# Kernel tuning notes

Measured on AMD Instinct MI355X. Metric: run time of the kernel, lower is better.

The kernel has to match this reference:

```python
import jax, jax.numpy as jnp
import numpy as np

T, B, I, H, K = 200, 2048, 128, 128, 4


def setup_inputs() -> dict:
    key = jax.random.key(0)
    ks = jax.random.split(key, 7)
    inputs = jax.random.normal(ks[0], (T, B, I), jnp.float32)
    lengths = jax.random.randint(ks[1], (B,), 1, T + 1, jnp.int32)
    si = 1.0 / np.sqrt(I)
    sh = 1.0 / np.sqrt(H)
    w0 = jax.random.uniform(ks[2], (H,), jnp.float32, -sh, sh)      # Linear(H,1,bias=False)
    w1_w = jax.random.uniform(ks[3], (H, I), jnp.float32, -si, si)  # Linear(I,H)
    w1_b = jax.random.uniform(ks[4], (H,), jnp.float32, -si, si)
    w2_w = jax.random.uniform(ks[5], (H, I), jnp.float32, -si, si)  # Linear(I,H,bias=False)
    w3_w = jax.random.uniform(ks[6], (H, I), jnp.float32, -si, si)  # Linear(I,H,bias=False)
    return dict(inputs=inputs, lengths=lengths, label_len=4,
                w0=w0, w1_w=w1_w, w1_b=w1_b, w2_w=w2_w, w3_w=w3_w)


def reference(inputs, lengths, label_len, w0, w1_w, w1_b, w2_w, w3_w):
    # inputs: [T, B, I] time-major padded sequences; lengths: [B]
    T_, B_, _ = inputs.shape
    Kl = label_len
    dt = inputs.dtype
    # packed semantics: padded positions are exactly zero
    valid = (jnp.arange(T_)[:, None] < lengths[None, :])  # [T, B]
    x = inputs * valid[..., None].astype(dt)
    x1 = x @ w1_w.T + w1_b                                 # [T, B, H]
    x2 = x @ w2_w.T                                        # [T, B, H]
    # running mean m_s[t] = mean(inputs[:t+1]) (zeros at padding, as in torch)
    m_s = jnp.cumsum(x, axis=0) / jnp.arange(1, T_ + 1, dtype=dt)[:, None, None]
    # labeled timesteps: last min(L, label_len) steps of each sequence
    start = jnp.maximum(lengths - Kl, 0)                   # [B]
    t_lab = start[:, None] + jnp.arange(Kl)[None, :]       # [B, K]
    lab_valid = t_lab < lengths[:, None]                   # [B, K]
    t_c = jnp.minimum(t_lab, T_ - 1)
    b_idx = jnp.arange(B_)[:, None]
    x2_lab = x2[t_c, b_idx]                                # [B, K, H]
    wms_lab = m_s[t_c, b_idx] @ w3_w.T                     # [B, K, H]
    c = x2_lab + wms_lab                                   # [B, K, H]
    # att[b,k,s] = w0 . sigmoid(x1[s,b] + x2[t_k,b] + wms[t_k,b])
    att = jnp.einsum('sbkh,h->bks',
                     jax.nn.sigmoid(x1[:, :, None, :] + c[None, :, :, :]), w0)
    causal = (jnp.arange(T_)[None, None, :] <= t_lab[:, :, None]) & lab_valid[:, :, None]
    att = att * causal.astype(dt)                          # [B, K, T]
    h = jnp.einsum('bks,sbh->bkh', att, x1) + x2_lab       # [B, K, H]
    return h * lab_valid[..., None].astype(dt)
```

## Files before the change

kernel.cpp:

```cpp
#include <hip/hip_runtime.h>
#include <stdint.h>

#define T_DIM 200
#define B_DIM 2048
#define I_DIM 128
#define H_DIM 128
#define TS    32

typedef float  f32x4  __attribute__((ext_vector_type(4)));
typedef __bf16 bf16x8 __attribute__((ext_vector_type(8)));

union BF8 { ushort4 u2[2]; bf16x8 v; };

static __device__ __forceinline__ unsigned short f2bf(float f) {
    union { __bf16 b; unsigned short u; } c; c.b = (__bf16)f; return c.u;
}
static __device__ __forceinline__ float bf2f(unsigned short s) {
    union { unsigned u; float f; } c; c.u = ((unsigned)s) << 16;
    return c.f;
}
static __device__ __forceinline__ ushort4 cvt4(float4 v) {
    return make_ushort4(f2bf(v.x), f2bf(v.y), f2bf(v.z), f2bf(v.w));
}

static __device__ __forceinline__ int ekbase(int h) {
    return (h << 3) ^ ((h >> 4) << 3);
}

__global__ __launch_bounds__(256, 4) void fused_kernel(
    const float* __restrict__ x, const int* __restrict__ lengths,
    const float* __restrict__ w0, const float* __restrict__ w1,
    const float* __restrict__ b1, const float* __restrict__ w2,
    const float* __restrict__ w3, float* __restrict__ out,
    unsigned* __restrict__ wq)
{
    __shared__ __align__(16) unsigned short xs[TS][136];
    __shared__ __align__(16) unsigned short x1s[TS][130];
    __shared__ __align__(16) float attp[TS][36];
    __shared__ __align__(16) float attk[TS][4];
    __shared__ __align__(16) float ektS2[H_DIM * 8];
    __shared__ __align__(16) float x2ls[4][H_DIM];
    __shared__ __align__(16) unsigned short axl[4][136];
    __shared__ __align__(16) unsigned short ams[4][136];
    __shared__ int b_sh;

    const int tid  = threadIdx.x;
    const int lane = tid & 63;
    const int wv   = tid >> 6;
    const int l15  = lane & 15;
    const int quad = lane >> 4;

    if (tid < 128) ektS2[ekbase(tid) + 4] = w0[tid];

    bf16x8 bfr[2][4];
    float  bias[2];
    #pragma unroll
    for (int nt = 0; nt < 2; ++nt) {
        const int n = wv * 32 + nt * 16 + l15;
        bias[nt] = b1[n];
        #pragma unroll
        for (int ks = 0; ks < 4; ++ks) {
            const int kc = ks * 32 + quad * 8;
            const float4 p0 = *(const float4*)(w1 + (size_t)n * I_DIM + kc);
            const float4 p1 = *(const float4*)(w1 + (size_t)n * I_DIM + kc + 4);
            BF8 t;
            t.u2[0] = cvt4(p0);
            t.u2[1] = cvt4(p1);
            bfr[nt][ks] = t.v;
        }
    }

    const int sr0 = tid >> 5;
    const int sf4 = tid & 31;
    const int i   = tid & 127;
    const int hcol = tid & 127;
    const int half = tid >> 7;
    const int rE  = wv * 8 + (lane >> 3);
    const int hE0 = (lane & 7) * 16;

    int bprev = -1;
    for (;;) {
        int b;
        if (wq) {
            if (tid == 0) b_sh = (int)atomicAdd(wq, 1u);
            __syncthreads();
            b = b_sh;
        } else {
            if (bprev >= 0) break;
            b = blockIdx.x;
        }
        if (b >= B_DIM) break;
        bprev = b;

        const int L     = lengths[b];
        const int start = (L > 4) ? (L - 4) : 0;
        const int nv    = (L < 4) ? L : 4;

        const float* xp = x + (size_t)b * I_DIM + i;
        float v0 = 0.f, v1 = 0.f, v2 = 0.f, v3 = 0.f;
        if (tid < 128) {
            v0 = xp[(size_t)(start + 0) * (B_DIM * I_DIM)];
            v1 = xp[(size_t)(start + 1) * (B_DIM * I_DIM)];
            v2 = xp[(size_t)(start + 2) * (B_DIM * I_DIM)];
            v3 = xp[(size_t)(start + 3) * (B_DIM * I_DIM)];
        }

        {
            const float* xq = x + (size_t)b * I_DIM + sf4 * 4;
            const size_t RS = (size_t)B_DIM * I_DIM;
            f32x4 s0 = (f32x4){0.f, 0.f, 0.f, 0.f};
            f32x4 s1 = s0, s2 = s0, s3 = s0;
            int t = sr0;
            for (; t + 24 < start; t += 32) {
                s0 += *(const f32x4*)(xq + (size_t)(t     ) * RS);
                s1 += *(const f32x4*)(xq + (size_t)(t +  8) * RS);
                s2 += *(const f32x4*)(xq + (size_t)(t + 16) * RS);
                s3 += *(const f32x4*)(xq + (size_t)(t + 24) * RS);
            }
            for (; t < start; t += 8)
                s0 += *(const f32x4*)(xq + (size_t)t * RS);
            const f32x4 s = (s0 + s1) + (s2 + s3);
            float* psum = &attp[0][0];
            *(f32x4*)&psum[sr0 * 132 + sf4 * 4] = s;
        }
        __syncthreads();

        if (tid < 128) {
            const float* psum = &attp[0][0];
            float p = 0.f;
            #pragma unroll
            for (int g = 0; g < 8; ++g) p += psum[g * 132 + i];
            const float p0 = p + v0, p1 = p0 + v1, p2 = p1 + v2, p3 = p2 + v3;
            axl[0][i] = f2bf(v0); axl[1][i] = f2bf(v1);
            axl[2][i] = f2bf(v2); axl[3][i] = f2bf(v3);
            ams[0][i] = f2bf(p0 / (float)(start + 1));
            ams[1][i] = f2bf(p1 / (float)(start + 2));
            ams[2][i] = f2bf(p2 / (float)(start + 3));
            ams[3][i] = f2bf(p3 / (float)(start + 4));
        }
        __syncthreads();

        #pragma unroll
        for (int nt = 0; nt < 2; ++nt) {
            const int n = wv * 32 + nt * 16 + l15;
            f32x4 c1 = (f32x4){0.f, 0.f, 0.f, 0.f};
            f32x4 c2 = (f32x4){0.f, 0.f, 0.f, 0.f};
            #pragma unroll
            for (int ks = 0; ks < 4; ++ks) {
                const int kc = ks * 32 + quad * 8;
                const bf16x8 a1 = *(const bf16x8*)&axl[l15 & 3][kc];
                const bf16x8 a2 = *(const bf16x8*)&ams[l15 & 3][kc];
                const float4 q0 = *(const float4*)(w2 + (size_t)n * I_DIM + kc);
                const float4 q1 = *(const float4*)(w2 + (size_t)n * I_DIM + kc + 4);
                const float4 r0 = *(const float4*)(w3 + (size_t)n * I_DIM + kc);
                const float4 r1 = *(const float4*)(w3 + (size_t)n * I_DIM + kc + 4);
                BF8 bw2, bw3;
                bw2.u2[0] = cvt4(q0); bw2.u2[1] = cvt4(q1);
                bw3.u2[0] = cvt4(r0); bw3.u2[1] = cvt4(r1);
                c1 = __builtin_amdgcn_mfma_f32_16x16x32_bf16(a1, bw2.v, c1, 0, 0, 0);
                c2 = __builtin_amdgcn_mfma_f32_16x16x32_bf16(a2, bw3.v, c2, 0, 0, 0);
            }
            if (quad == 0) {
                const int eb = ekbase(n);
                #pragma unroll
                for (int r = 0; r < 4; ++r) {
                    x2ls[r][n] = c1[r];
                    ektS2[eb + r] = __builtin_amdgcn_exp2f(-1.44269504f * (c1[r] + c2[r]));
                }
            }
        }
        __syncthreads();

        float hacc0 = 0.f, hacc1 = 0.f, hacc2v = 0.f, hacc3 = 0.f;

        for (int t0 = 0; t0 < L; t0 += TS) {
            const int nrows = (L - t0 < TS) ? (L - t0) : TS;

            #pragma unroll
            for (int it = 0; it < 4; ++it) {
                const int sl = tid + it * 256;
                const int r = sl >> 5, f4 = sl & 31;
                ushort4 w = make_ushort4(0, 0, 0, 0);
                if (r < nrows) {
                    const float4 v = *(const float4*)(
                        x + ((size_t)(t0 + r) * B_DIM + b) * I_DIM + f4 * 4);
                    w = cvt4(v);
                }
                *(ushort4*)&xs[r][f4 * 4] = w;
            }
            __syncthreads();

            #pragma unroll
            for (int mt = 0; mt < 2; ++mt) {
                bf16x8 afr[4];
                #pragma unroll
                for (int ks = 0; ks < 4; ++ks)
                    afr[ks] = *(const bf16x8*)&xs[mt * 16 + l15][ks * 32 + quad * 8];
                #pragma unroll
                for (int nt = 0; nt < 2; ++nt) {
                    f32x4 acc = (f32x4){0.f, 0.f, 0.f, 0.f};
                    #pragma unroll
                    for (int ks = 0; ks < 4; ++ks)
                        acc = __builtin_amdgcn_mfma_f32_16x16x32_bf16(
                            afr[ks], bfr[nt][ks], acc, 0, 0, 0);
                    const int h = wv * 32 + nt * 16 + l15;
                    const int tr = mt * 16 + quad * 4;
                    #pragma unroll
                    for (int r = 0; r < 4; ++r)
                        x1s[tr + r][h] = f2bf(acc[r] + bias[nt]);
                }
            }
            __syncthreads();

            {
                f32x4 a = (f32x4){0.f, 0.f, 0.f, 0.f};
                #pragma unroll
                for (int hh = 0; hh < 16; hh += 2) {
                    const int ha = hE0 + hh;
                    const unsigned xv2 = *(const unsigned*)&x1s[rE][ha];
                    const float xa = bf2f((unsigned short)(xv2 & 0xFFFFu));
                    const float xb = bf2f((unsigned short)(xv2 >> 16));
                    const float Ea = __builtin_amdgcn_exp2f(-1.44269504f * xa);
                    const float Eb = __builtin_amdgcn_exp2f(-1.44269504f * xb);
                    const int eba = ekbase(ha), ebb = ekbase(ha + 1);
                    const f32x4 eka = *(const f32x4*)&ektS2[eba];
                    const f32x4 ekb = *(const f32x4*)&ektS2[ebb];
                    const float wa = ektS2[eba + 4], wb = ektS2[ebb + 4];
                    #pragma unroll
                    for (int k = 0; k < 4; ++k)
                        a[k] += wa * __builtin_amdgcn_rcpf(1.f + Ea * eka[k])
                              + wb * __builtin_amdgcn_rcpf(1.f + Eb * ekb[k]);
                }
                #pragma unroll
                for (int m = 1; m <= 4; m <<= 1)
                    #pragma unroll
                    for (int k = 0; k < 4; ++k)
                        a[k] += __shfl_xor(a[k], m);
                if ((lane & 7) == 0) {
                    const int s = t0 + rE;
                    f32x4 o;
                    o[0] = (0 < nv && s <= start    ) ? a[0] : 0.f;
                    o[1] = (1 < nv && s <= start + 1) ? a[1] : 0.f;
                    o[2] = (2 < nv && s <= start + 2) ? a[2] : 0.f;
                    o[3] = (3 < nv && s <= start + 3) ? a[3] : 0.f;
                    *(f32x4*)&attk[rE][0] = o;
                }
            }
            __syncthreads();

            {
                const int sbase = half * 16;
                #pragma unroll
                for (int s2 = 0; s2 < 16; ++s2) {
                    const int srow = sbase + s2;
                    const f32x4 a4 = *(const f32x4*)&attk[srow][0];
                    const float xv = bf2f(x1s[srow][hcol]);
                    hacc0 += a4[0] * xv; hacc1 += a4[1] * xv;
                    hacc2v += a4[2] * xv; hacc3 += a4[3] * xv;
                }
            }
        }

        {
            float* h2 = &attp[0][0];
            if (half == 1) {
                *(f32x4*)&h2[hcol * 4] = (f32x4){hacc0, hacc1, hacc2v, hacc3};
            }
            __syncthreads();
            if (tid < 128) {
                const f32x4 o = *(const f32x4*)&h2[hcol * 4];
                hacc0 += o[0]; hacc1 += o[1]; hacc2v += o[2]; hacc3 += o[3];
                out[((size_t)b * 4 + 0) * H_DIM + hcol] = (0 < nv) ? hacc0 + x2ls[0][hcol] : 0.f;
                out[((size_t)b * 4 + 1) * H_DIM + hcol] = (1 < nv) ? hacc1 + x2ls[1][hcol] : 0.f;
                out[((size_t)b * 4 + 2) * H_DIM + hcol] = (2 < nv) ? hacc2v + x2ls[2][hcol] : 0.f;
                out[((size_t)b * 4 + 3) * H_DIM + hcol] = (3 < nv) ? hacc3 + x2ls[3][hcol] : 0.f;
            }
        }
    }
}

extern "C" void kernel_launch(void* const* d_in, const int* in_sizes, int n_in,
                              void* d_out, int out_size, void* d_ws, size_t ws_size,
                              hipStream_t stream) {
    (void)in_sizes; (void)n_in; (void)out_size;
    const float* x       = (const float*)d_in[0];
    const int*   lengths = (const int*)d_in[1];
    const float* w0 = (const float*)d_in[3];
    const float* w1 = (const float*)d_in[4];
    const float* b1 = (const float*)d_in[5];
    const float* w2 = (const float*)d_in[6];
    const float* w3 = (const float*)d_in[7];
    float* out = (float*)d_out;

    unsigned* wq = (d_ws != nullptr && ws_size >= sizeof(unsigned))
                       ? (unsigned*)d_ws : nullptr;
    if (wq) {
        hipMemsetAsync(wq, 0, sizeof(unsigned), stream);
        fused_kernel<<<dim3(1280), 256, 0, stream>>>(
            x, lengths, w0, w1, b1, w2, w3, out, wq);
    } else {
        fused_kernel<<<dim3(B_DIM), 256, 0, stream>>>(
            x, lengths, w0, w1, b1, w2, w3, out, nullptr);
    }
}
```

Before: 386.7 us.

## Replace atomic work-queue persistent blocks with one block per batch element

Result: faster. 353.2 us (-8.6%).

```diff
diff --git a/kernel.cpp b/kernel.cpp
--- a/kernel.cpp
+++ b/kernel.cpp
@@ -31,8 +31,7 @@
     const float* __restrict__ x, const int* __restrict__ lengths,
     const float* __restrict__ w0, const float* __restrict__ w1,
     const float* __restrict__ b1, const float* __restrict__ w2,
-    const float* __restrict__ w3, float* __restrict__ out,
-    unsigned* __restrict__ wq)
+    const float* __restrict__ w3, float* __restrict__ out)
 {
     __shared__ __align__(16) unsigned short xs[TS][136];
     __shared__ __align__(16) unsigned short x1s[TS][130];
@@ -42,15 +41,28 @@
     __shared__ __align__(16) float x2ls[4][H_DIM];
     __shared__ __align__(16) unsigned short axl[4][136];
     __shared__ __align__(16) unsigned short ams[4][136];
-    __shared__ int b_sh;
-
+
+    const int b    = blockIdx.x;
     const int tid  = threadIdx.x;
     const int lane = tid & 63;
     const int wv   = tid >> 6;
     const int l15  = lane & 15;
     const int quad = lane >> 4;
+    const int L     = lengths[b];
+    const int start = (L > 4) ? (L - 4) : 0;
+    const int nv    = (L < 4) ? L : 4;
 
     if (tid < 128) ektS2[ekbase(tid) + 4] = w0[tid];
+
+    const int i = tid & 127;
+    const float* xp = x + (size_t)b * I_DIM + i;
+    float v0 = 0.f, v1 = 0.f, v2 = 0.f, v3 = 0.f;
+    if (tid < 128) {
+        v0 = xp[(size_t)(start + 0) * (B_DIM * I_DIM)];
+        v1 = xp[(size_t)(start + 1) * (B_DIM * I_DIM)];
+        v2 = xp[(size_t)(start + 2) * (B_DIM * I_DIM)];
+        v3 = xp[(size_t)(start + 3) * (B_DIM * I_DIM)];
+    }
 
     bf16x8 bfr[2][4];
     float  bias[2];
@@ -72,209 +84,179 @@
 
     const int sr0 = tid >> 5;
     const int sf4 = tid & 31;
-    const int i   = tid & 127;
+    {
+        const float* xq = x + (size_t)b * I_DIM + sf4 * 4;
+        const size_t RS = (size_t)B_DIM * I_DIM;
+        f32x4 s0 = (f32x4){0.f, 0.f, 0.f, 0.f};
+        f32x4 s1 = s0, s2 = s0, s3 = s0;
+        int t = sr0;
+        for (; t + 24 < start; t += 32) {
+            s0 += *(const f32x4*)(xq + (size_t)(t     ) * RS);
+            s1 += *(const f32x4*)(xq + (size_t)(t +  8) * RS);
+            s2 += *(const f32x4*)(xq + (size_t)(t + 16) * RS);
+            s3 += *(const f32x4*)(xq + (size_t)(t + 24) * RS);
+        }
+        for (; t < start; t += 8)
+            s0 += *(const f32x4*)(xq + (size_t)t * RS);
+        const f32x4 s = (s0 + s1) + (s2 + s3);
+        float* psum = &attp[0][0];
+        *(f32x4*)&psum[sr0 * 132 + sf4 * 4] = s;
+    }
+    __syncthreads();
+
+    if (tid < 128) {
+        const float* psum = &attp[0][0];
+        float p = 0.f;
+        #pragma unroll
+        for (int g = 0; g < 8; ++g) p += psum[g * 132 + i];
+        const float p0 = p + v0, p1 = p0 + v1, p2 = p1 + v2, p3 = p2 + v3;
+        axl[0][i] = f2bf(v0); axl[1][i] = f2bf(v1);
+        axl[2][i] = f2bf(v2); axl[3][i] = f2bf(v3);
+        ams[0][i] = f2bf(p0 / (float)(start + 1));
+        ams[1][i] = f2bf(p1 / (float)(start + 2));
+        ams[2][i] = f2bf(p2 / (float)(start + 3));
+        ams[3][i] = f2bf(p3 / (float)(start + 4));
+    }
+    __syncthreads();
+
+    #pragma unroll
+    for (int nt = 0; nt < 2; ++nt) {
+        const int n = wv * 32 + nt * 16 + l15;
+        f32x4 c1 = (f32x4){0.f, 0.f, 0.f, 0.f};
+        f32x4 c2 = (f32x4){0.f, 0.f, 0.f, 0.f};
+        #pragma unroll
+        for (int ks = 0; ks < 4; ++ks) {
+            const int kc = ks * 32 + quad * 8;
+            const bf16x8 a1 = *(const bf16x8*)&axl[l15 & 3][kc];
+            const bf16x8 a2 = *(const bf16x8*)&ams[l15 & 3][kc];
+            const float4 q0 = *(const float4*)(w2 + (size_t)n * I_DIM + kc);
+            const float4 q1 = *(const float4*)(w2 + (size_t)n * I_DIM + kc + 4);
+            const float4 r0 = *(const float4*)(w3 + (size_t)n * I_DIM + kc);
+            const float4 r1 = *(const float4*)(w3 + (size_t)n * I_DIM + kc + 4);
+            BF8 bw2, bw3;
+            bw2.u2[0] = cvt4(q0); bw2.u2[1] = cvt4(q1);
+            bw3.u2[0] = cvt4(r0); bw3.u2[1] = cvt4(r1);
+            c1 = __builtin_amdgcn_mfma_f32_16x16x32_bf16(a1, bw2.v, c1, 0, 0, 0);
+            c2 = __builtin_amdgcn_mfma_f32_16x16x32_bf16(a2, bw3.v, c2, 0, 0, 0);
+        }
+        if (quad == 0) {
+            const int eb = ekbase(n);
+            #pragma unroll
+            for (int r = 0; r < 4; ++r) {
+                x2ls[r][n] = c1[r];
+                ektS2[eb + r] = __builtin_amdgcn_exp2f(-1.44269504f * (c1[r] + c2[r]));
+            }
+        }
+    }
+    __syncthreads();
+
     const int hcol = tid & 127;
     const int half = tid >> 7;
     const int rE  = wv * 8 + (lane >> 3);
     const int hE0 = (lane & 7) * 16;
-
-    int bprev = -1;
-    for (;;) {
-        int b;
-        if (wq) {
-            if (tid == 0) b_sh = (int)atomicAdd(wq, 1u);
-            __syncthreads();
-            b = b_sh;
-        } else {
-            if (bprev >= 0) break;
-            b = blockIdx.x;
-        }
-        if (b >= B_DIM) break;
-        bprev = b;
-
-        const int L     = lengths[b];
-        const int start = (L > 4) ? (L - 4) : 0;
-        const int nv    = (L < 4) ? L : 4;
-
-        const float* xp = x + (size_t)b * I_DIM + i;
-        float v0 = 0.f, v1 = 0.f, v2 = 0.f, v3 = 0.f;
+    float hacc0 = 0.f, hacc1 = 0.f, hacc2v = 0.f, hacc3 = 0.f;
+
+    for (int t0 = 0; t0 < L; t0 += TS) {
+        const int nrows = (L - t0 < TS) ? (L - t0) : TS;
+
+        #pragma unroll
+        for (int it = 0; it < 4; ++it) {
+            const int sl = tid + it * 256;
+            const int r = sl >> 5, f4 = sl & 31;
+            ushort4 w = make_ushort4(0, 0, 0, 0);
+            if (r < nrows) {
+                const float4 v = *(const float4*)(
+                    x + ((size_t)(t0 + r) * B_DIM + b) * I_DIM + f4 * 4);
+                w = cvt4(v);
+            }
+            *(ushort4*)&xs[r][f4 * 4] = w;
+        }
+        __syncthreads();
+
+        #pragma unroll
+        for (int mt = 0; mt < 2; ++mt) {
+            bf16x8 afr[4];
+            #pragma unroll
+            for (int ks = 0; ks < 4; ++ks)
+                afr[ks] = *(const bf16x8*)&xs[mt * 16 + l15][ks * 32 + quad * 8];
+            #pragma unroll
+            for (int nt = 0; nt < 2; ++nt) {
+                f32x4 acc = (f32x4){0.f, 0.f, 0.f, 0.f};
+                #pragma unroll
+                for (int ks = 0; ks < 4; ++ks)
+                    acc = __builtin_amdgcn_mfma_f32_16x16x32_bf16(
+                        afr[ks], bfr[nt][ks], acc, 0, 0, 0);
+                const int h = wv * 32 + nt * 16 + l15;
+                const int tr = mt * 16 + quad * 4;
+                #pragma unroll
+                for (int r = 0; r < 4; ++r)
+                    x1s[tr + r][h] = f2bf(acc[r] + bias[nt]);
+            }
+        }
+        __syncthreads();
+
+        {
+            f32x4 a = (f32x4){0.f, 0.f, 0.f, 0.f};
+            #pragma unroll
+            for (int hh = 0; hh < 16; hh += 2) {
+                const int ha = hE0 + hh;
+                const unsigned xv2 = *(const unsigned*)&x1s[rE][ha];
+                const float xa = bf2f((unsigned short)(xv2 & 0xFFFFu));
+                const float xb = bf2f((unsigned short)(xv2 >> 16));
+                const float Ea = __builtin_amdgcn_exp2f(-1.44269504f * xa);
+                const float Eb = __builtin_amdgcn_exp2f(-1.44269504f * xb);
+                const int eba = ekbase(ha), ebb = ekbase(ha + 1);
+                const f32x4 eka = *(const f32x4*)&ektS2[eba];
+                const f32x4 ekb = *(const f32x4*)&ektS2[ebb];
+                const float wa = ektS2[eba + 4], wb = ektS2[ebb + 4];
+                #pragma unroll
+                for (int k = 0; k < 4; ++k)
+                    a[k] += wa * __builtin_amdgcn_rcpf(1.f + Ea * eka[k])
+                          + wb * __builtin_amdgcn_rcpf(1.f + Eb * ekb[k]);
+            }
+            #pragma unroll
+            for (int m = 1; m <= 4; m <<= 1)
+                #pragma unroll
+                for (int k = 0; k < 4; ++k)
+                    a[k] += __shfl_xor(a[k], m);
+            if ((lane & 7) == 0) {
+                const int s = t0 + rE;
+                f32x4 o;
+                o[0] = (0 < nv && s <= start    ) ? a[0] : 0.f;
+                o[1] = (1 < nv && s <= start + 1) ? a[1] : 0.f;
+                o[2] = (2 < nv && s <= start + 2) ? a[2] : 0.f;
+                o[3] = (3 < nv && s <= start + 3) ? a[3] : 0.f;
+                *(f32x4*)&attk[rE][0] = o;
+            }
+        }
+        __syncthreads();
+
+        {
+            const int sbase = half * 16;
+            #pragma unroll
+            for (int s2 = 0; s2 < 16; ++s2) {
+                const int srow = sbase + s2;
+                const f32x4 a4 = *(const f32x4*)&attk[srow][0];
+                const float xv = bf2f(x1s[srow][hcol]);
+                hacc0 += a4[0] * xv; hacc1 += a4[1] * xv;
+                hacc2v += a4[2] * xv; hacc3 += a4[3] * xv;
+            }
+        }
+    }
+
+    {
+        float* h2 = &attp[0][0];
+        if (half == 1) {
+            *(f32x4*)&h2[hcol * 4] = (f32x4){hacc0, hacc1, hacc2v, hacc3};
+        }
+        __syncthreads();
         if (tid < 128) {
-            v0 = xp[(size_t)(start + 0) * (B_DIM * I_DIM)];
-            v1 = xp[(size_t)(start + 1) * (B_DIM * I_DIM)];
-            v2 = xp[(size_t)(start + 2) * (B_DIM * I_DIM)];
-            v3 = xp[(size_t)(start + 3) * (B_DIM * I_DIM)];
-        }
-
-        {
-            const float* xq = x + (size_t)b * I_DIM + sf4 * 4;
-            const size_t RS = (size_t)B_DIM * I_DIM;
-            f32x4 s0 = (f32x4){0.f, 0.f, 0.f, 0.f};
-            f32x4 s1 = s0, s2 = s0, s3 = s0;
-            int t = sr0;
-            for (; t + 24 < start; t += 32) {
-                s0 += *(const f32x4*)(xq + (size_t)(t     ) * RS);
-                s1 += *(const f32x4*)(xq + (size_t)(t +  8) * RS);
-                s2 += *(const f32x4*)(xq + (size_t)(t + 16) * RS);
-                s3 += *(const f32x4*)(xq + (size_t)(t + 24) * RS);
-            }
-            for (; t < start; t += 8)
-                s0 += *(const f32x4*)(xq + (size_t)t * RS);
-            const f32x4 s = (s0 + s1) + (s2 + s3);
-            float* psum = &attp[0][0];
-            *(f32x4*)&psum[sr0 * 132 + sf4 * 4] = s;
-        }
-        __syncthreads();
-
-        if (tid < 128) {
-            const float* psum = &attp[0][0];
-            float p = 0.f;
-            #pragma unroll
-            for (int g = 0; g < 8; ++g) p += psum[g * 132 + i];
-            const float p0 = p + v0, p1 = p0 + v1, p2 = p1 + v2, p3 = p2 + v3;
-            axl[0][i] = f2bf(v0); axl[1][i] = f2bf(v1);
-            axl[2][i] = f2bf(v2); axl[3][i] = f2bf(v3);
-            ams[0][i] = f2bf(p0 / (float)(start + 1));
-            ams[1][i] = f2bf(p1 / (float)(start + 2));
-            ams[2][i] = f2bf(p2 / (float)(start + 3));
-            ams[3][i] = f2bf(p3 / (float)(start + 4));
-        }
-        __syncthreads();
-
-        #pragma unroll
-        for (int nt = 0; nt < 2; ++nt) {
-            const int n = wv * 32 + nt * 16 + l15;
-            f32x4 c1 = (f32x4){0.f, 0.f, 0.f, 0.f};
-            f32x4 c2 = (f32x4){0.f, 0.f, 0.f, 0.f};
-            #pragma unroll
-            for (int ks = 0; ks < 4; ++ks) {
-                const int kc = ks * 32 + quad * 8;
-                const bf16x8 a1 = *(const bf16x8*)&axl[l15 & 3][kc];
-                const bf16x8 a2 = *(const bf16x8*)&ams[l15 & 3][kc];
-                const float4 q0 = *(const float4*)(w2 + (size_t)n * I_DIM + kc);
-                const float4 q1 = *(const float4*)(w2 + (size_t)n * I_DIM + kc + 4);
-                const float4 r0 = *(const float4*)(w3 + (size_t)n * I_DIM + kc);
-                const float4 r1 = *(const float4*)(w3 + (size_t)n * I_DIM + kc + 4);
-                BF8 bw2, bw3;
-                bw2.u2[0] = cvt4(q0); bw2.u2[1] = cvt4(q1);
-                bw3.u2[0] = cvt4(r0); bw3.u2[1] = cvt4(r1);
-                c1 = __builtin_amdgcn_mfma_f32_16x16x32_bf16(a1, bw2.v, c1, 0, 0, 0);
-                c2 = __builtin_amdgcn_mfma_f32_16x16x32_bf16(a2, bw3.v, c2, 0, 0, 0);
-            }
-            if (quad == 0) {
-                const int eb = ekbase(n);
-                #pragma unroll
-                for (int r = 0; r < 4; ++r) {
-                    x2ls[r][n] = c1[r];
-                    ektS2[eb + r] = __builtin_amdgcn_exp2f(-1.44269504f * (c1[r] + c2[r]));
-                }
-            }
-        }
-        __syncthreads();
-
-        float hacc0 = 0.f, hacc1 = 0.f, hacc2v = 0.f, hacc3 = 0.f;
-
-        for (int t0 = 0; t0 < L; t0 += TS) {
-            const int nrows = (L - t0 < TS) ? (L - t0) : TS;
-
-            #pragma unroll
-            for (int it = 0; it < 4; ++it) {
-                const int sl = tid + it * 256;
-                const int r = sl >> 5, f4 = sl & 31;
-                ushort4 w = make_ushort4(0, 0, 0, 0);
-                if (r < nrows) {
-                    const float4 v = *(const float4*)(
-                        x + ((size_t)(t0 + r) * B_DIM + b) * I_DIM + f4 * 4);
-                    w = cvt4(v);
-                }
-                *(ushort4*)&xs[r][f4 * 4] = w;
-            }
-            __syncthreads();
-
-            #pragma unroll
-            for (int mt = 0; mt < 2; ++mt) {
-                bf16x8 afr[4];
-                #pragma unroll
-                for (int ks = 0; ks < 4; ++ks)
-                    afr[ks] = *(const bf16x8*)&xs[mt * 16 + l15][ks * 32 + quad * 8];
-                #pragma unroll
-                for (int nt = 0; nt < 2; ++nt) {
-                    f32x4 acc = (f32x4){0.f, 0.f, 0.f, 0.f};
-                    #pragma unroll
-                    for (int ks = 0; ks < 4; ++ks)
-                        acc = __builtin_amdgcn_mfma_f32_16x16x32_bf16(
-                            afr[ks], bfr[nt][ks], acc, 0, 0, 0);
-                    const int h = wv * 32 + nt * 16 + l15;
-                    const int tr = mt * 16 + quad * 4;
-                    #pragma unroll
-                    for (int r = 0; r < 4; ++r)
-                        x1s[tr + r][h] = f2bf(acc[r] + bias[nt]);
-                }
-            }
-            __syncthreads();
-
-            {
-                f32x4 a = (f32x4){0.f, 0.f, 0.f, 0.f};
-                #pragma unroll
-                for (int hh = 0; hh < 16; hh += 2) {
-                    const int ha = hE0 + hh;
-                    const unsigned xv2 = *(const unsigned*)&x1s[rE][ha];
-                    const float xa = bf2f((unsigned short)(xv2 & 0xFFFFu));
-                    const float xb = bf2f((unsigned short)(xv2 >> 16));
-                    const float Ea = __builtin_amdgcn_exp2f(-1.44269504f * xa);
-                    const float Eb = __builtin_amdgcn_exp2f(-1.44269504f * xb);
-                    const int eba = ekbase(ha), ebb = ekbase(ha + 1);
-                    const f32x4 eka = *(const f32x4*)&ektS2[eba];
-                    const f32x4 ekb = *(const f32x4*)&ektS2[ebb];
-                    const float wa = ektS2[eba + 4], wb = ektS2[ebb + 4];
-                    #pragma unroll
-                    for (int k = 0; k < 4; ++k)
-                        a[k] += wa * __builtin_amdgcn_rcpf(1.f + Ea * eka[k])
-                              + wb * __builtin_amdgcn_rcpf(1.f + Eb * ekb[k]);
-                }
-                #pragma unroll
-                for (int m = 1; m <= 4; m <<= 1)
-                    #pragma unroll
-                    for (int k = 0; k < 4; ++k)
-                        a[k] += __shfl_xor(a[k], m);
-                if ((lane & 7) == 0) {
-                    const int s = t0 + rE;
-                    f32x4 o;
-                    o[0] = (0 < nv && s <= start    ) ? a[0] : 0.f;
-                    o[1] = (1 < nv && s <= start + 1) ? a[1] : 0.f;
-                    o[2] = (2 < nv && s <= start + 2) ? a[2] : 0.f;
-                    o[3] = (3 < nv && s <= start + 3) ? a[3] : 0.f;
-                    *(f32x4*)&attk[rE][0] = o;
-                }
-            }
-            __syncthreads();
-
-            {
-                const int sbase = half * 16;
-                #pragma unroll
-                for (int s2 = 0; s2 < 16; ++s2) {
-                    const int srow = sbase + s2;
-                    const f32x4 a4 = *(const f32x4*)&attk[srow][0];
-                    const float xv = bf2f(x1s[srow][hcol]);
-                    hacc0 += a4[0] * xv; hacc1 += a4[1] * xv;
-                    hacc2v += a4[2] * xv; hacc3 += a4[3] * xv;
-                }
-            }
-        }
-
-        {
-            float* h2 = &attp[0][0];
-            if (half == 1) {
-                *(f32x4*)&h2[hcol * 4] = (f32x4){hacc0, hacc1, hacc2v, hacc3};
-            }
-            __syncthreads();
-            if (tid < 128) {
-                const f32x4 o = *(const f32x4*)&h2[hcol * 4];
-                hacc0 += o[0]; hacc1 += o[1]; hacc2v += o[2]; hacc3 += o[3];
-                out[((size_t)b * 4 + 0) * H_DIM + hcol] = (0 < nv) ? hacc0 + x2ls[0][hcol] : 0.f;
-                out[((size_t)b * 4 + 1) * H_DIM + hcol] = (1 < nv) ? hacc1 + x2ls[1][hcol] : 0.f;
-                out[((size_t)b * 4 + 2) * H_DIM + hcol] = (2 < nv) ? hacc2v + x2ls[2][hcol] : 0.f;
-                out[((size_t)b * 4 + 3) * H_DIM + hcol] = (3 < nv) ? hacc3 + x2ls[3][hcol] : 0.f;
-            }
+            const f32x4 o = *(const f32x4*)&h2[hcol * 4];
+            hacc0 += o[0]; hacc1 += o[1]; hacc2v += o[2]; hacc3 += o[3];
+            out[((size_t)b * 4 + 0) * H_DIM + hcol] = (0 < nv) ? hacc0 + x2ls[0][hcol] : 0.f;
+            out[((size_t)b * 4 + 1) * H_DIM + hcol] = (1 < nv) ? hacc1 + x2ls[1][hcol] : 0.f;
+            out[((size_t)b * 4 + 2) * H_DIM + hcol] = (2 < nv) ? hacc2v + x2ls[2][hcol] : 0.f;
+            out[((size_t)b * 4 + 3) * H_DIM + hcol] = (3 < nv) ? hacc3 + x2ls[3][hcol] : 0.f;
         }
     }
 }
@@ -282,7 +264,7 @@
 extern "C" void kernel_launch(void* const* d_in, const int* in_sizes, int n_in,
                               void* d_out, int out_size, void* d_ws, size_t ws_size,
                               hipStream_t stream) {
-    (void)in_sizes; (void)n_in; (void)out_size;
+    (void)in_sizes; (void)n_in; (void)out_size; (void)d_ws; (void)ws_size;
     const float* x       = (const float*)d_in[0];
     const int*   lengths = (const int*)d_in[1];
     const float* w0 = (const float*)d_in[3];
@@ -292,14 +274,5 @@
     const float* w3 = (const float*)d_in[7];
     float* out = (float*)d_out;
 
-    unsigned* wq = (d_ws != nullptr && ws_size >= sizeof(unsigned))
-                       ? (unsigned*)d_ws : nullptr;
-    if (wq) {
-        hipMemsetAsync(wq, 0, sizeof(unsigned), stream);
-        fused_kernel<<<dim3(1280), 256, 0, stream>>>(
-            x, lengths, w0, w1, b1, w2, w3, out, wq);
-    } else {
-        fused_kernel<<<dim3(B_DIM), 256, 0, stream>>>(
-            x, lengths, w0, w1, b1, w2, w3, out, nullptr);
-    }
-}
+    fused_kernel<<<dim3(B_DIM), 256, 0, stream>>>(x, lengths, w0, w1, b1, w2, w3, out);
+}
```
